# Kernel tuning notes

Measured on AMD Instinct MI355X. Metric: run time of the kernel, lower is better.

The kernel has to match this reference:

```python
import jax, jax.numpy as jnp
import numpy as np

# Winograd F(2x2, 3x3) transform matrices
B = jnp.array([[1.0, 0.0, 0.0, 0.0],
               [0.0, 1.0, -1.0, 1.0],
               [-1.0, 1.0, 1.0, 0.0],
               [0.0, 0.0, 0.0, -1.0]], dtype=jnp.float32)
G = jnp.array([[1.0, 0.0, 0.0],
               [0.5, 0.5, 0.5],
               [0.5, -0.5, 0.5],
               [0.0, 0.0, 1.0]], dtype=jnp.float32)
A = jnp.array([[1.0, 0.0],
               [1.0, 1.0],
               [1.0, -1.0],
               [0.0, -1.0]], dtype=jnp.float32)

PADDING = 1


def setup_inputs() -> dict:
    key = jax.random.key(0)
    k1, k2 = jax.random.split(key)
    x = jax.random.normal(k1, (16, 128, 56, 56), dtype=jnp.float32)
    kernel = jax.random.normal(k2, (128, 128, 3, 3), dtype=jnp.float32) * 0.05
    return {"x": x, "kernel": kernel}


def _winograd_fwd(x, kernel):
    # Pad input
    x = jnp.pad(x, ((0, 0), (0, 0), (PADDING, PADDING), (PADDING, PADDING)))
    N, C, H, W = x.shape
    a, overlap, m = 4, 2, 2  # tile size, stride, output tile
    Th = (H - a) // overlap + 1
    Tw = (W - a) // overlap + 1
    H_out, W_out = H - 2, W - 2

    # Filter transform: U = G @ g @ G^T  -> (K, C, 4, 4)
    U = jnp.einsum('ij,kcjl,ml->kcim', G, kernel, G)

    # Extract overlapping 4x4 tiles with stride 2: (N, C, Th, Tw, 4, 4)
    ii = (jnp.arange(Th) * overlap)[:, None] + jnp.arange(a)[None, :]  # (Th, 4)
    jj = (jnp.arange(Tw) * overlap)[:, None] + jnp.arange(a)[None, :]  # (Tw, 4)
    d = x[:, :, ii]               # (N, C, Th, 4, W)
    d = d[:, :, :, :, jj]         # (N, C, Th, 4, Tw, 4)
    d = d.transpose(0, 1, 2, 4, 3, 5)  # (N, C, Th, Tw, 4, 4)

    # Input transform: V = B^T @ d @ B
    V = jnp.einsum('ji,nchwjk,kl->nchwil', B, d, B)  # (N, C, Th, Tw, 4, 4)

    # Elementwise multiply + channel reduction: (N, K, Th, Tw, 4, 4)
    M = jnp.einsum('kcij,nchwij->nkhwij', U, V)

    # Output transform: Y_tile = A^T @ M @ A -> (N, K, Th, Tw, 2, 2)
    Yt = jnp.einsum('ji,nkhwjl,lm->nkhwim', A, M, A)

    # Reassemble tiles into (N, K, H_out, W_out)
    Y = Yt.transpose(0, 1, 2, 4, 3, 5).reshape(N, Yt.shape[1], H_out, W_out)
    return Y


def reference(x, kernel):
    return _winograd_fwd(x, kernel)
```

## Files before the change

kernel.cpp:

```cpp
#include <hip/hip_runtime.h>
#include <hip/hip_bf16.h>

typedef __attribute__((ext_vector_type(8))) short bf16x8;
typedef __attribute__((ext_vector_type(16))) float f32x16;
typedef __attribute__((ext_vector_type(4))) unsigned int u32x4;

#define CC 128
#define KK 128
#define HH 56
#define WW 56
#define HW (HH * WW)

__device__ __forceinline__ unsigned short f2bf(float f) {
  unsigned int u = __builtin_bit_cast(unsigned int, f);
  u += 0x7FFFu + ((u >> 16) & 1u);
  return (unsigned short)(u >> 16);
}

__global__ void wtrans_kernel(const float* __restrict__ kin,
                              unsigned short* __restrict__ wt2) {
  int idx = blockIdx.x * 256 + threadIdx.x;
  int j = idx & 7;
  int l = (idx >> 3) & 63;
  int kf = (idx >> 9) & 1;
  int kp = (idx >> 10) & 1;
  int cs = (idx >> 11) & 3;
  int m = idx >> 13;
  int ch = (m >= 9) ? 1 : 0;
  int rs = m - ch * 9;
  int k = kp * 64 + kf * 32 + (l & 31);
  int c = ch * 64 + cs * 16 + (l >> 5) * 8 + j;
  wt2[idx] = f2bf(kin[(k * CC + c) * 9 + rs]);
}

__global__ __launch_bounds__(512, 2) void conv_kernel(
    const float* __restrict__ x, const unsigned short* __restrict__ wt2,
    float* __restrict__ out) {
  __shared__ __align__(16) unsigned char xs[6 * 58 * 128];

  const int tid = threadIdx.x;
  const int lane = tid & 63;
  const int wv = tid >> 6;
  const int bh = blockIdx.x;
  const int n = blockIdx.y;
  const int r0 = bh * 4;

  const int p = lane & 31;
  const int dr = p >> 3;
  const int dw = p & 7;
  const int hi = lane >> 5;

  const int kp = wv >> 2;
  const int sh = wv & 3;
  const int ns = (sh == 3) ? 1 : 2;
  const int s0 = sh * 2;

  f32x16 acc[2][2] = {};

  const int gw = lane - 1;
  const bool wok = (gw >= 0) && (gw < WW);

  auto stage = [&](int ch) {
    const int oct = wv;
    const float* xb = x + ((size_t)n * CC + (ch * 64 + oct * 8)) * HW + gw;
#pragma unroll
    for (int lr = 0; lr < 6; ++lr) {
      const int gh = r0 - 1 + lr;
      const bool ok = wok && (gh >= 0) && (gh < HH);
      const float* xp = xb + gh * WW;
      unsigned int q0, q1, q2, q3;
      {
        float v0 = ok ? xp[0 * HW] : 0.f;
        float v1 = ok ? xp[1 * HW] : 0.f;
        float v2 = ok ? xp[2 * HW] : 0.f;
        float v3 = ok ? xp[3 * HW] : 0.f;
        float v4 = ok ? xp[4 * HW] : 0.f;
        float v5 = ok ? xp[5 * HW] : 0.f;
        float v6 = ok ? xp[6 * HW] : 0.f;
        float v7 = ok ? xp[7 * HW] : 0.f;
        q0 = (unsigned int)f2bf(v0) | ((unsigned int)f2bf(v1) << 16);
        q1 = (unsigned int)f2bf(v2) | ((unsigned int)f2bf(v3) << 16);
        q2 = (unsigned int)f2bf(v4) | ((unsigned int)f2bf(v5) << 16);
        q3 = (unsigned int)f2bf(v6) | ((unsigned int)f2bf(v7) << 16);
      }
      if (lane < 58) {
        const int rec = lr * 58 + lane;
        u32x4 qq = {q0, q1, q2, q3};
        *(u32x4*)(xs + (rec << 7) + ((oct ^ (lane & 7)) << 4)) = qq;
      }
    }
  };

  auto loadA = [&](int m, int i) -> bf16x8 {
    return *(const bf16x8*)(wt2 +
                            ((((m * 4 + (i >> 1)) * 2 + kp) * 2 + (i & 1)) << 9) +
                            (lane << 3));
  };

  stage(0);
  __syncthreads();

  bf16x8 ac[8], an[8];
#pragma unroll
  for (int i = 0; i < 8; ++i) ac[i] = loadA(0, i);

#pragma unroll 1
  for (int m = 0; m < 18; ++m) {
    if (m == 9) {
      __syncthreads();
      stage(1);
      __syncthreads();
    }
    const int mn = (m < 17) ? m + 1 : 17;
#pragma unroll
    for (int i = 0; i < 8; ++i) an[i] = loadA(mn, i);

    const int rs = (m >= 9) ? m - 9 : m;
    const int fr = (rs * 11) >> 5;
    const int fs = rs - fr * 3;
    const int lw7 = (dw + fs) & 7;
    const int rbase = ((dr + fr) * 58 + dw + fs) << 7;

#pragma unroll
    for (int cs = 0; cs < 4; ++cs) {
      const int sbase = rbase + ((((cs << 1) + hi) ^ lw7) << 4);
#pragma unroll
      for (int si = 0; si < 2; ++si) {
        if (si < ns) {
          bf16x8 b = *(const bf16x8*)(xs + sbase + (s0 + si) * 1024);
          acc[0][si] = __builtin_amdgcn_mfma_f32_32x32x16_bf16(ac[cs * 2 + 0], b,
                                                               acc[0][si], 0, 0, 0);
          acc[1][si] = __builtin_amdgcn_mfma_f32_32x32x16_bf16(ac[cs * 2 + 1], b,
                                                               acc[1][si], 0, 0, 0);
        }
      }
    }
#pragma unroll
    for (int i = 0; i < 8; ++i) ac[i] = an[i];
  }

#pragma unroll
  for (int kf = 0; kf < 2; ++kf) {
#pragma unroll
    for (int si = 0; si < 2; ++si) {
      if (si < ns) {
        const int s = s0 + si;
#pragma unroll
        for (int r = 0; r < 16; ++r) {
          const int krow = kp * 64 + kf * 32 + (r & 3) + ((r >> 2) << 3) + (hi << 2);
          out[(((size_t)n * KK + krow) * HH + (r0 + dr)) * WW + s * 8 + dw] =
              acc[kf][si][r];
        }
      }
    }
  }
}

extern "C" void kernel_launch(void* const* d_in, const int* in_sizes, int n_in,
                              void* d_out, int out_size, void* d_ws, size_t ws_size,
                              hipStream_t stream) {
  const float* x = (const float*)d_in[0];
  const float* kin = (const float*)d_in[1];
  float* out = (float*)d_out;
  unsigned short* wt2 = (unsigned short*)d_ws;

  hipLaunchKernelGGL(wtrans_kernel, dim3(576), dim3(256), 0, stream, kin, wt2);
  hipLaunchKernelGGL(conv_kernel, dim3(14, 16), dim3(512), 0, stream, x, wt2, out);
}
```

Measured before the change: 37.07 us.

## Prepack input to padded bf16 layout and stream both halves into LDS asynchronously

Adds a prepack kernel that converts x to bf16 in a zero-padded, channel-octet-interleaved layout in workspace. The conv kernel then issues direct global-to-LDS loads for both channel halves up front, into a double-sized LDS buffer, and waits on only the first half before computing. This removes the in-kernel fp32 gather, convert and LDS store, and overlaps loading of the second half with the first compute phase. The cost is an extra kernel launch and a full round trip of the prepacked input through memory. The larger LDS footprint may also reduce occupancy.

```diff
diff --git a/kernel.cpp b/kernel.cpp
--- a/kernel.cpp
+++ b/kernel.cpp
@@ -3,7 +3,6 @@
 
 typedef __attribute__((ext_vector_type(8))) short bf16x8;
 typedef __attribute__((ext_vector_type(16))) float f32x16;
-typedef __attribute__((ext_vector_type(4))) unsigned int u32x4;
 
 #define CC 128
 #define KK 128
@@ -11,10 +10,19 @@
 #define WW 56
 #define HW (HH * WW)
 
+#define WT_OFF 0
+#define XP_OFF (512 * 1024)
+
 __device__ __forceinline__ unsigned short f2bf(float f) {
   unsigned int u = __builtin_bit_cast(unsigned int, f);
   u += 0x7FFFu + ((u >> 16) & 1u);
   return (unsigned short)(u >> 16);
+}
+
+__device__ __forceinline__ void gload_lds16(const void* g, void* l) {
+  __builtin_amdgcn_global_load_lds((__attribute__((address_space(1))) void*)g,
+                                   (__attribute__((address_space(3))) void*)l,
+                                   16, 0, 0);
 }
 
 __global__ void wtrans_kernel(const float* __restrict__ kin,
@@ -22,21 +30,38 @@
   int idx = blockIdx.x * 256 + threadIdx.x;
   int j = idx & 7;
   int l = (idx >> 3) & 63;
-  int kf = (idx >> 9) & 1;
-  int kp = (idx >> 10) & 1;
+  int kf = (idx >> 9) & 3;
   int cs = (idx >> 11) & 3;
   int m = idx >> 13;
   int ch = (m >= 9) ? 1 : 0;
   int rs = m - ch * 9;
-  int k = kp * 64 + kf * 32 + (l & 31);
+  int k = kf * 32 + (l & 31);
   int c = ch * 64 + cs * 16 + (l >> 5) * 8 + j;
   wt2[idx] = f2bf(kin[(k * CC + c) * 9 + rs]);
 }
 
+__global__ void prepack_kernel(const float* __restrict__ x,
+                               unsigned short* __restrict__ xp) {
+  int idx = blockIdx.x * 256 + threadIdx.x;
+  int w = idx & 63;
+  int r = idx >> 6;
+  int h = r % 58;
+  int t = r / 58;
+  bool ok = (w >= 1) && (w <= 56) && (h >= 1) && (h <= 56);
+  const float* src = x + (size_t)t * 8 * HW + (h - 1) * WW + (w - 1);
+  unsigned short o[8];
+#pragma unroll
+  for (int ci = 0; ci < 8; ++ci) {
+    float v = ok ? src[ci * HW] : 0.f;
+    o[ci] = f2bf(v);
+  }
+  *(bf16x8*)(xp + (size_t)idx * 8) = *(bf16x8*)o;
+}
+
 __global__ __launch_bounds__(512, 2) void conv_kernel(
-    const float* __restrict__ x, const unsigned short* __restrict__ wt2,
+    const unsigned short* __restrict__ xp, const unsigned short* __restrict__ wt2,
     float* __restrict__ out) {
-  __shared__ __align__(16) unsigned char xs[6 * 58 * 128];
+  __shared__ __align__(16) unsigned char xs[2 * 6 * 64 * 128];
 
   const int tid = threadIdx.x;
   const int lane = tid & 63;
@@ -55,101 +80,83 @@
   const int ns = (sh == 3) ? 1 : 2;
   const int s0 = sh * 2;
 
+  {
+    const int oct = (lane & 7) ^ ((lane >> 3) & 7);
+    const int col = wv * 8 + (lane >> 3);
+    const unsigned short* g0 =
+        xp + ((((size_t)n * 16 + oct) * 58 + r0) * 64 + col) * 8;
+#pragma unroll
+    for (int ch = 0; ch < 2; ++ch) {
+#pragma unroll
+      for (int lr = 0; lr < 6; ++lr) {
+        gload_lds16(g0 + ch * (8 * 58 * 64 * 8) + lr * 512,
+                    xs + ch * 49152 + lr * 8192 + wv * 1024);
+      }
+    }
+  }
+
   f32x16 acc[2][2] = {};
+  bf16x8 A0[8], A1[8];
 
-  const int gw = lane - 1;
-  const bool wok = (gw >= 0) && (gw < WW);
+  auto ldA = [&](int step, bf16x8* D) {
+#pragma unroll
+    for (int cs = 0; cs < 4; ++cs)
+#pragma unroll
+      for (int kfl = 0; kfl < 2; ++kfl)
+        D[cs * 2 + kfl] = *(const bf16x8*)(
+            wt2 + (((step * 4 + cs) * 4 + kp * 2 + kfl) << 9) + lane * 8);
+  };
 
-  auto stage = [&](int ch) {
-    const int oct = wv;
-    const float* xb = x + ((size_t)n * CC + (ch * 64 + oct * 8)) * HW + gw;
+  asm volatile("s_waitcnt vmcnt(6)" ::: "memory");
+  __builtin_amdgcn_s_barrier();
+  asm volatile("" ::: "memory");
+
+  ldA(0, A0);
+
+  auto phase = [&](const int ch, const unsigned char* buf) {
 #pragma unroll
-    for (int lr = 0; lr < 6; ++lr) {
-      const int gh = r0 - 1 + lr;
-      const bool ok = wok && (gh >= 0) && (gh < HH);
-      const float* xp = xb + gh * WW;
-      unsigned int q0, q1, q2, q3;
-      {
-        float v0 = ok ? xp[0 * HW] : 0.f;
-        float v1 = ok ? xp[1 * HW] : 0.f;
-        float v2 = ok ? xp[2 * HW] : 0.f;
-        float v3 = ok ? xp[3 * HW] : 0.f;
-        float v4 = ok ? xp[4 * HW] : 0.f;
-        float v5 = ok ? xp[5 * HW] : 0.f;
-        float v6 = ok ? xp[6 * HW] : 0.f;
-        float v7 = ok ? xp[7 * HW] : 0.f;
-        q0 = (unsigned int)f2bf(v0) | ((unsigned int)f2bf(v1) << 16);
-        q1 = (unsigned int)f2bf(v2) | ((unsigned int)f2bf(v3) << 16);
-        q2 = (unsigned int)f2bf(v4) | ((unsigned int)f2bf(v5) << 16);
-        q3 = (unsigned int)f2bf(v6) | ((unsigned int)f2bf(v7) << 16);
-      }
-      if (lane < 58) {
-        const int rec = lr * 58 + lane;
-        u32x4 qq = {q0, q1, q2, q3};
-        *(u32x4*)(xs + (rec << 7) + ((oct ^ (lane & 7)) << 4)) = qq;
+    for (int rs = 0; rs < 9; ++rs) {
+      const int step = ch * 9 + rs;
+      bf16x8* Ac = (step & 1) ? A1 : A0;
+      bf16x8* An = (step & 1) ? A0 : A1;
+      if (step < 17) ldA(step + 1, An);
+      const int fr = (rs * 11) >> 5;
+      const int fs = rs - fr * 3;
+      const int rbase = ((dr + fr) * 64 + dw + fs) << 7;
+      const int xr = (dw + fs) & 7;
+#pragma unroll
+      for (int cs = 0; cs < 4; ++cs) {
+        const int sb = rbase + ((((cs << 1) + hi) ^ xr) << 4);
+#pragma unroll
+        for (int si = 0; si < 2; ++si) {
+          if (si < ns) {
+            bf16x8 b = *(const bf16x8*)(buf + sb + (s0 + si) * 1024);
+            acc[0][si] = __builtin_amdgcn_mfma_f32_32x32x16_bf16(
+                Ac[cs * 2 + 0], b, acc[0][si], 0, 0, 0);
+            acc[1][si] = __builtin_amdgcn_mfma_f32_32x32x16_bf16(
+                Ac[cs * 2 + 1], b, acc[1][si], 0, 0, 0);
+          }
+        }
       }
     }
   };
 
-  auto loadA = [&](int m, int i) -> bf16x8 {
-    return *(const bf16x8*)(wt2 +
-                            ((((m * 4 + (i >> 1)) * 2 + kp) * 2 + (i & 1)) << 9) +
-                            (lane << 3));
-  };
-
-  stage(0);
+  phase(0, xs);
   __syncthreads();
-
-  bf16x8 ac[8], an[8];
-#pragma unroll
-  for (int i = 0; i < 8; ++i) ac[i] = loadA(0, i);
-
-#pragma unroll 1
-  for (int m = 0; m < 18; ++m) {
-    if (m == 9) {
-      __syncthreads();
-      stage(1);
-      __syncthreads();
-    }
-    const int mn = (m < 17) ? m + 1 : 17;
-#pragma unroll
-    for (int i = 0; i < 8; ++i) an[i] = loadA(mn, i);
-
-    const int rs = (m >= 9) ? m - 9 : m;
-    const int fr = (rs * 11) >> 5;
-    const int fs = rs - fr * 3;
-    const int lw7 = (dw + fs) & 7;
-    const int rbase = ((dr + fr) * 58 + dw + fs) << 7;
+  phase(1, xs + 49152);
 
 #pragma unroll
-    for (int cs = 0; cs < 4; ++cs) {
-      const int sbase = rbase + ((((cs << 1) + hi) ^ lw7) << 4);
-#pragma unroll
-      for (int si = 0; si < 2; ++si) {
-        if (si < ns) {
-          bf16x8 b = *(const bf16x8*)(xs + sbase + (s0 + si) * 1024);
-          acc[0][si] = __builtin_amdgcn_mfma_f32_32x32x16_bf16(ac[cs * 2 + 0], b,
-                                                               acc[0][si], 0, 0, 0);
-          acc[1][si] = __builtin_amdgcn_mfma_f32_32x32x16_bf16(ac[cs * 2 + 1], b,
-                                                               acc[1][si], 0, 0, 0);
-        }
-      }
-    }
-#pragma unroll
-    for (int i = 0; i < 8; ++i) ac[i] = an[i];
-  }
-
-#pragma unroll
-  for (int kf = 0; kf < 2; ++kf) {
+  for (int kfl = 0; kfl < 2; ++kfl) {
 #pragma unroll
     for (int si = 0; si < 2; ++si) {
       if (si < ns) {
         const int s = s0 + si;
 #pragma unroll
         for (int r = 0; r < 16; ++r) {
-          const int krow = kp * 64 + kf * 32 + (r & 3) + ((r >> 2) << 3) + (hi << 2);
+          const int krow =
+              kp * 64 + kfl * 32 + (r & 3) + ((r >> 2) << 3) + (hi << 2);
           out[(((size_t)n * KK + krow) * HH + (r0 + dr)) * WW + s * 8 + dw] =
-              acc[kf][si][r];
+              acc[kfl][si][r];
         }
       }
     }
@@ -162,8 +169,10 @@
   const float* x = (const float*)d_in[0];
   const float* kin = (const float*)d_in[1];
   float* out = (float*)d_out;
-  unsigned short* wt2 = (unsigned short*)d_ws;
+  unsigned short* wt2 = (unsigned short*)((char*)d_ws + WT_OFF);
+  unsigned short* xp = (unsigned short*)((char*)d_ws + XP_OFF);
 
+  hipLaunchKernelGGL(prepack_kernel, dim3(3712), dim3(256), 0, stream, x, xp);
   hipLaunchKernelGGL(wtrans_kernel, dim3(576), dim3(256), 0, stream, kin, wt2);
-  hipLaunchKernelGGL(conv_kernel, dim3(14, 16), dim3(512), 0, stream, x, wt2, out);
+  hipLaunchKernelGGL(conv_kernel, dim3(14, 16), dim3(512), 0, stream, xp, wt2, out);
 }
```

New measurement: 37.70 us. No clear change (+1.7%).
